# Kernel optimization log

Hardware: AMD Instinct MI355X
Metric: run time of the kernel (lower is better)

## Reference

```python
import jax, jax.numpy as jnp
import numpy as np

NEG_SLOPE = 0.1


def _conv3d(x, w, b):
    # standard 3x3x3 conv, stride 1, pad 1, NCDHW layout
    y = jax.lax.conv_general_dilated(
        x, w, window_strides=(1, 1, 1), padding=[(1, 1), (1, 1), (1, 1)],
        dimension_numbers=('NCDHW', 'OIDHW', 'NCDHW'))
    return y + b[None, :, None, None, None]


def _deform_conv3d_hw(x, w_off, b_off, w, b):
    """DeformConvPack_d with dimension='HW': 3x3x3 conv whose H/W sampling
    positions are shifted by learned per-location offsets (bilinear sample in
    H,W; integer taps in D). Zero padding outside the volume."""
    B, C, D, H, W = x.shape
    # offset conv: 2 offsets (dh, dw) per kernel tap, 27 taps -> 54 channels
    off = _conv3d(x, w_off, b_off).reshape(B, 27, 2, D, H, W)
    x_flat = x.reshape(B, C, D * H * W)
    d_grid = jnp.arange(D)[:, None, None]          # [D,1,1]
    h_grid = jnp.arange(H)[None, :, None]          # [1,H,1]
    w_grid = jnp.arange(W)[None, None, :]          # [1,1,W]
    out = jnp.zeros((B, w.shape[0], D, H, W), x.dtype)
    k = 0
    for kd in (-1, 0, 1):
        pd = d_grid + kd                            # integer depth tap
        valid_d = (pd >= 0) & (pd < D)
        pdc = jnp.clip(pd, 0, D - 1)
        for kh in (-1, 0, 1):
            for kw in (-1, 0, 1):
                ph = h_grid + kh + off[:, k, 0]     # [B,D,H,W] float
                pw = w_grid + kw + off[:, k, 1]
                h0 = jnp.floor(ph)
                w0 = jnp.floor(pw)
                th = ph - h0                        # bilinear fracs
                tw = pw - w0
                h0i = h0.astype(jnp.int32)
                w0i = w0.astype(jnp.int32)
                samp = jnp.zeros((B, C, D, H, W), x.dtype)
                for dh, wgt_h in ((0, 1.0 - th), (1, th)):
                    hh = h0i + dh
                    vh = (hh >= 0) & (hh < H)
                    hhc = jnp.clip(hh, 0, H - 1)
                    for dw, wgt_w in ((0, 1.0 - tw), (1, tw)):
                        ww = w0i + dw
                        v = valid_d & vh & (ww >= 0) & (ww < W)
                        wwc = jnp.clip(ww, 0, W - 1)
                        idx = (pdc * H + hhc) * W + wwc          # [B,D,H,W]
                        g = jnp.take_along_axis(
                            x_flat, idx.reshape(B, 1, D * H * W), axis=2
                        ).reshape(B, C, D, H, W)
                        wgt = jnp.where(v, wgt_h * wgt_w, 0.0)
                        samp = samp + g * wgt[:, None]
                # accumulate this tap's contribution through the conv weight
                out = out + jnp.einsum('bcdhw,oc->bodhw', samp,
                                       w[:, :, kd + 1, kh + 1, kw + 1])
                k += 1
    return out + b[None, :, None, None, None]


def setup_inputs() -> dict:
    key = jax.random.key(0)
    ks = jax.random.split(key, 9)
    B, nf, D, H, W = 4, 48, 12, 56, 56
    fan = 1.0 / np.sqrt(nf * 27)
    x = jax.random.normal(ks[0], (B, nf, D, H, W), jnp.float32)
    # offset convs: small weights so sampled offsets stay O(1) pixel
    w_off0 = jax.random.normal(ks[1], (54, nf, 3, 3, 3), jnp.float32) * 0.01
    b_off0 = jax.random.normal(ks[2], (54,), jnp.float32) * 0.01
    w0 = jax.random.normal(ks[3], (nf, nf, 3, 3, 3), jnp.float32) * fan
    b0 = jax.random.normal(ks[4], (nf,), jnp.float32) * 0.01
    w_off1 = jax.random.normal(ks[5], (54, nf, 3, 3, 3), jnp.float32) * 0.01
    b_off1 = jax.random.normal(ks[6], (54,), jnp.float32) * 0.01
    w1 = jax.random.normal(ks[7], (nf, nf, 3, 3, 3), jnp.float32) * fan
    b1 = jax.random.normal(ks[8], (nf,), jnp.float32) * 0.01
    return {"x": x, "w_off0": w_off0, "b_off0": b_off0, "w0": w0, "b0": b0,
            "w_off1": w_off1, "b_off1": b_off1, "w1": w1, "b1": b1}


def reference(x, w_off0, b_off0, w0, b0, w_off1, b_off1, w1, b1):
    h = _deform_conv3d_hw(x, w_off0, b_off0, w0, b0)
    h = jnp.where(h >= 0, h, NEG_SLOPE * h)  # LeakyReLU(0.1)
    y = _deform_conv3d_hw(h, w_off1, b_off1, w1, b1)
    return y + x
```

## Files before the change

kernel.cpp:

```cpp
#include <hip/hip_runtime.h>
#include <hip/hip_bf16.h>

constexpr int B_ = 4, C_ = 48, D_ = 12, H_ = 56, W_ = 56;
constexpr int DHW_ = D_ * H_ * W_;
constexpr int NLOC_ = B_ * DHW_;
constexpr int OFFC_ = 54;
constexpr int NXCD_ = 8;

typedef short bf16x8 __attribute__((ext_vector_type(8)));
typedef float f32x4  __attribute__((ext_vector_type(4)));
typedef float f32x2  __attribute__((ext_vector_type(2)));
typedef unsigned int u32x4 __attribute__((ext_vector_type(4)));
typedef unsigned int u32x2 __attribute__((ext_vector_type(2)));

__device__ __forceinline__ int xcd_swizzle(int bid, int nwg) {
    int xcd = bid % NXCD_, lid = bid / NXCD_;
    int q = nwg / NXCD_, r = nwg % NXCD_;
    return (xcd < r ? xcd * (q + 1) : r * (q + 1) + (xcd - r) * q) + lid;
}

__device__ __forceinline__ unsigned int f2bf_u(float f) {
    __hip_bfloat16 h = __float2bfloat16(f);
    return (unsigned int)__builtin_bit_cast(unsigned short, h);
}

__device__ __forceinline__ f32x2 bfpair(unsigned int pv) {
    f32x2 r;
    r.x = __builtin_bit_cast(float, pv << 16);
    r.y = __builtin_bit_cast(float, pv & 0xffff0000u);
    return r;
}
__device__ __forceinline__ f32x2 pk_mul(f32x2 a, f32x2 b) {
    f32x2 d;
    asm("v_pk_mul_f32 %0, %1, %2" : "=v"(d) : "v"(a), "v"(b));
    return d;
}
__device__ __forceinline__ f32x2 pk_fma(f32x2 a, f32x2 b, f32x2 c) {
    f32x2 d;
    asm("v_pk_fma_f32 %0, %1, %2, %3" : "=v"(d) : "v"(a), "v"(b), "v"(c));
    return d;
}
__device__ __forceinline__ unsigned int cvt_pk_bf16(float lo, float hi) {
    unsigned int r;
    asm("v_cvt_pk_bf16_f32 %0, %1, %2" : "=v"(r) : "v"(lo), "v"(hi));
    return r;
}

__device__ __forceinline__ u32x4 interp4_pk(u32x4 c00, u32x4 c01, u32x4 c10, u32x4 c11,
                                            f32x2 w0, f32x2 w1, f32x2 w2, f32x2 w3) {
    u32x4 pv;
#pragma unroll
    for (int u = 0; u < 4; ++u) {
        f32x2 r = pk_mul(w0, bfpair(c00[u]));
        r = pk_fma(w1, bfpair(c01[u]), r);
        r = pk_fma(w2, bfpair(c10[u]), r);
        r = pk_fma(w3, bfpair(c11[u]), r);
        pv[u] = cvt_pk_bf16(r.x, r.y);
    }
    return pv;
}

__global__ void __launch_bounds__(256) repack_frag_kernel(
    const float* __restrict__ w, unsigned short* __restrict__ wf, int OC, int MT) {
    int t = blockIdx.x * 256 + threadIdx.x;
    int total = 27 * MT * 1024;
    if (t >= total) return;
    int i    = t & 7;
    int lane = (t >> 3) & 63;
    int ks   = (t >> 9) & 1;
    int mt   = (t >> 10) % MT;
    int k    = t / (MT << 10);
    int oc = mt * 16 + (lane & 15);
    int c  = ks * 32 + 8 * (lane >> 4) + i;
    float v = (oc < OC && c < 48) ? w[((size_t)oc * 48 + c) * 27 + k] : 0.0f;
    wf[t] = (unsigned short)f2bf_u(v);
}

__global__ void __launch_bounds__(256) to_cl_kernel(const float* __restrict__ x,
                                                    unsigned short* __restrict__ xcl) {
    int loc = blockIdx.x * 256 + threadIdx.x;
    int b = loc / DHW_, s = loc - b * DHW_;
    const float* xp = x + (size_t)b * (C_ * DHW_) + s;
#pragma unroll
    for (int q = 0; q < 6; ++q) {
        float v[8];
#pragma unroll
        for (int u = 0; u < 8; ++u) v[u] = xp[(size_t)(q * 8 + u) * DHW_];
        u32x4 o;
#pragma unroll
        for (int u = 0; u < 4; ++u)
            o[u] = cvt_pk_bf16(v[2 * u], v[2 * u + 1]);
        *(u32x4*)(xcl + ((size_t)q * NLOC_ + loc) * 8) = o;
    }
}

__global__ void __launch_bounds__(128) offconv_mfma(
    const unsigned short* __restrict__ xcl,
    const unsigned short* __restrict__ wf,
    const float* __restrict__ bo,
    float* __restrict__ off) {
    __shared__ unsigned short S[2][64][64];
    int tid = threadIdx.x, wid = tid >> 6, lane = tid & 63;
    int base = xcd_swizzle(blockIdx.x, gridDim.x) * 64;
    int loc = base + lane;
    int b = loc / DHW_;
    int sp = loc - b * DHW_;
    int w = sp % W_; int t1 = sp / W_;
    int h = t1 % H_; int d = t1 / H_;
    int g = lane >> 4, li = lane & 15, l7 = lane & 7;

    u32x4 z = {0, 0, 0, 0};
    *(u32x4*)&S[wid][lane][(6 ^ l7) * 8] = z;
    *(u32x4*)&S[wid][lane][(7 ^ l7) * 8] = z;

    f32x4 acc[4][4];
#pragma unroll
    for (int mt = 0; mt < 4; ++mt)
#pragma unroll
        for (int nt = 0; nt < 4; ++nt) acc[mt][nt] = (f32x4){0.f, 0.f, 0.f, 0.f};

    const u32x4* plane[6];
#pragma unroll
    for (int q = 0; q < 6; ++q)
        plane[q] = (const u32x4*)(xcl + ((size_t)q * NLOC_ + (size_t)b * DHW_) * 8);

#pragma unroll 1
    for (int i = 0; i < 14; ++i) {
        int k = wid + 2 * i;
        if (k >= 27) break;
        int kd = k / 9 - 1, kh = (k / 3) % 3 - 1, kw = k % 3 - 1;
        int pd = d + kd, ph = h + kh, pw = w + kw;
        bool valid = (pd >= 0) & (pd < D_) & (ph >= 0) & (ph < H_) & (pw >= 0) & (pw < W_);
        int pdc = min(max(pd, 0), D_ - 1);
        int phc = min(max(ph, 0), H_ - 1);
        int pwc = min(max(pw, 0), W_ - 1);
        int pix = (pdc * H_ + phc) * W_ + pwc;
        u32x4 pv[6];
#pragma unroll
        for (int cc = 0; cc < 6; ++cc) pv[cc] = plane[cc][pix];
#pragma unroll
        for (int cc = 0; cc < 6; ++cc) {
            if (!valid) pv[cc] = z;
            *(u32x4*)&S[wid][lane][(cc ^ l7) * 8] = pv[cc];
        }
        const unsigned short* wk = wf + (size_t)k * 4096 + lane * 8;
        bf16x8 a[4][2];
#pragma unroll
        for (int mt = 0; mt < 4; ++mt)
#pragma unroll
            for (int ks = 0; ks < 2; ++ks)
                a[mt][ks] = *(const bf16x8*)&wk[(mt * 2 + ks) * 512];
#pragma unroll
        for (int nt = 0; nt < 4; ++nt) {
            const unsigned short* sr = &S[wid][nt * 16 + li][0];
            bf16x8 b0 = *(const bf16x8*)&sr[((0 + g) ^ l7) * 8];
            bf16x8 b1 = *(const bf16x8*)&sr[((4 + g) ^ l7) * 8];
#pragma unroll
            for (int mt = 0; mt < 4; ++mt) {
                acc[mt][nt] = __builtin_amdgcn_mfma_f32_16x16x32_bf16(a[mt][0], b0, acc[mt][nt], 0, 0, 0);
                acc[mt][nt] = __builtin_amdgcn_mfma_f32_16x16x32_bf16(a[mt][1], b1, acc[mt][nt], 0, 0, 0);
            }
        }
    }

    float* XCH = (float*)&S[0][0][0];
    __syncthreads();
    if (wid == 1) {
#pragma unroll
        for (int mt = 0; mt < 2; ++mt)
#pragma unroll
            for (int nt = 0; nt < 4; ++nt)
                *(f32x4*)(XCH + (mt * 4 + nt) * 256 + lane * 4) = acc[mt][nt];
    }
    __syncthreads();
    if (wid == 0) {
#pragma unroll
        for (int mt = 0; mt < 2; ++mt)
#pragma unroll
            for (int nt = 0; nt < 4; ++nt)
                acc[mt][nt] += *(f32x4*)(XCH + (mt * 4 + nt) * 256 + lane * 4);
    }
    __syncthreads();
    if (wid == 1) {
#pragma unroll
        for (int mt = 2; mt < 4; ++mt)
#pragma unroll
            for (int nt = 0; nt < 4; ++nt)
                *(f32x4*)(XCH + ((mt - 2) * 4 + nt) * 256 + lane * 4) = acc[mt][nt];
    }
    __syncthreads();
    if (wid == 1) return;
#pragma unroll
    for (int mt = 2; mt < 4; ++mt)
#pragma unroll
        for (int nt = 0; nt < 4; ++nt)
            acc[mt][nt] += *(f32x4*)(XCH + ((mt - 2) * 4 + nt) * 256 + lane * 4);

    int s0 = base - b * DHW_;
#pragma unroll
    for (int mt = 0; mt < 4; ++mt) {
#pragma unroll
        for (int r = 0; r < 4; ++r) {
            int oc = mt * 16 + 4 * g + r;
            if (oc < OFFC_) {
                float bb = bo[oc];
#pragma unroll
                for (int nt = 0; nt < 4; ++nt) {
                    size_t addr = ((size_t)b * OFFC_ + oc) * DHW_ + (s0 + nt * 16 + li);
                    off[addr] = acc[mt][nt][r] + bb;
                }
            }
        }
    }
}

template <int LEAKY, int RESID, int CLOUT>
__global__ void __launch_bounds__(128) deform_mfma(
    const unsigned short* __restrict__ scl,
    const float* __restrict__ off,
    const unsigned short* __restrict__ wf,
    const float* __restrict__ bias,
    const float* __restrict__ resid,
    float* __restrict__ dstf,
    unsigned short* __restrict__ dstcl) {
    __shared__ unsigned short S[2][64][64];
    int tid = threadIdx.x, wid = tid >> 6, lane = tid & 63;
    int base = xcd_swizzle(blockIdx.x, gridDim.x) * 64;
    int loc = base + lane;
    int b = loc / DHW_;
    int sp = loc - b * DHW_;
    int w = sp % W_; int t1 = sp / W_;
    int h = t1 % H_; int d = t1 / H_;
    int g = lane >> 4, li = lane & 15, l7 = lane & 7;

    u32x4 z = {0, 0, 0, 0};
    *(u32x4*)&S[wid][lane][(6 ^ l7) * 8] = z;
    *(u32x4*)&S[wid][lane][(7 ^ l7) * 8] = z;

    f32x4 acc[3][4];
#pragma unroll
    for (int mt = 0; mt < 3; ++mt)
#pragma unroll
        for (int nt = 0; nt < 4; ++nt) acc[mt][nt] = (f32x4){0.f, 0.f, 0.f, 0.f};

    const u32x4* plane[6];
#pragma unroll
    for (int q = 0; q < 6; ++q)
        plane[q] = (const u32x4*)(scl + ((size_t)q * NLOC_ + (size_t)b * DHW_) * 8);
    const float* ob = off + (size_t)b * (OFFC_ * DHW_) + sp;

#pragma unroll 1
    for (int i = 0; i < 14; ++i) {
        int k = wid + 2 * i;
        if (k >= 27) break;
        int kd = k / 9 - 1, kh = (k / 3) % 3 - 1, kw = k % 3 - 1;
        int pd = d + kd;
        bool vd = (pd >= 0) & (pd < D_);
        int pdc = min(max(pd, 0), D_ - 1);

        float odh = ob[(size_t)(2 * k + 0) * DHW_];
        float odw = ob[(size_t)(2 * k + 1) * DHW_];
        float phf = (float)(h + kh) + odh;
        float pwf = (float)(w + kw) + odw;
        float h0f = floorf(phf), w0f = floorf(pwf);
        float th = phf - h0f, tw = pwf - w0f;
        int h0 = (int)h0f, w0 = (int)w0f;

        int pix[4];
        f32x4 cw;
#pragma unroll
        for (int dh = 0; dh < 2; ++dh) {
            int hh = h0 + dh;
            bool vh = vd & (hh >= 0) & (hh < H_);
            int hhc = min(max(hh, 0), H_ - 1);
            float wh = dh ? th : 1.0f - th;
#pragma unroll
            for (int dw = 0; dw < 2; ++dw) {
                int ww = w0 + dw;
                bool v = vh & (ww >= 0) & (ww < W_);
                int wwc = min(max(ww, 0), W_ - 1);
                float wwt = dw ? tw : 1.0f - tw;
                pix[dh * 2 + dw] = (pdc * H_ + hhc) * W_ + wwc;
                cw[dh * 2 + dw] = v ? wh * wwt : 0.0f;
            }
        }
        f32x2 w0p = {cw[0], cw[0]}, w1p = {cw[1], cw[1]};
        f32x2 w2p = {cw[2], cw[2]}, w3p = {cw[3], cw[3]};

#pragma unroll
        for (int half = 0; half < 2; ++half) {
            u32x4 st[3][4];
#pragma unroll
            for (int cc = 0; cc < 3; ++cc)
#pragma unroll
                for (int j = 0; j < 4; ++j)
                    st[cc][j] = plane[half * 3 + cc][pix[j]];
#pragma unroll
            for (int cc = 0; cc < 3; ++cc) {
                u32x4 pv = interp4_pk(st[cc][0], st[cc][1], st[cc][2], st[cc][3],
                                      w0p, w1p, w2p, w3p);
                *(u32x4*)&S[wid][lane][((half * 3 + cc) ^ l7) * 8] = pv;
            }
        }

        const unsigned short* wk = wf + (size_t)k * 3072 + lane * 8;
        bf16x8 a[3][2];
#pragma unroll
        for (int mt = 0; mt < 3; ++mt)
#pragma unroll
            for (int ks = 0; ks < 2; ++ks)
                a[mt][ks] = *(const bf16x8*)&wk[(mt * 2 + ks) * 512];
#pragma unroll
        for (int nt = 0; nt < 4; ++nt) {
            const unsigned short* sr = &S[wid][nt * 16 + li][0];
            bf16x8 b0 = *(const bf16x8*)&sr[((0 + g) ^ l7) * 8];
            bf16x8 b1 = *(const bf16x8*)&sr[((4 + g) ^ l7) * 8];
#pragma unroll
            for (int mt = 0; mt < 3; ++mt) {
                acc[mt][nt] = __builtin_amdgcn_mfma_f32_16x16x32_bf16(a[mt][0], b0, acc[mt][nt], 0, 0, 0);
                acc[mt][nt] = __builtin_amdgcn_mfma_f32_16x16x32_bf16(a[mt][1], b1, acc[mt][nt], 0, 0, 0);
            }
        }
    }

    float* XCH = (float*)&S[1][0][0];
    __syncthreads();
    if (wid == 1) {
#pragma unroll
        for (int mt = 0; mt < 2; ++mt)
#pragma unroll
            for (int nt = 0; nt < 4; ++nt)
                *(f32x4*)(XCH + (mt * 4 + nt) * 256 + lane * 4) = acc[mt][nt];
    }
    __syncthreads();
    if (wid == 0) {
#pragma unroll
        for (int mt = 0; mt < 2; ++mt)
#pragma unroll
            for (int nt = 0; nt < 4; ++nt)
                acc[mt][nt] += *(f32x4*)(XCH + (mt * 4 + nt) * 256 + lane * 4);
    }
    __syncthreads();
    if (wid == 1) {
#pragma unroll
        for (int nt = 0; nt < 4; ++nt)
            *(f32x4*)(XCH + nt * 256 + lane * 4) = acc[2][nt];
    }
    __syncthreads();
    if (wid == 1) return;
#pragma unroll
    for (int nt = 0; nt < 4; ++nt)
        acc[2][nt] += *(f32x4*)(XCH + nt * 256 + lane * 4);

    if (CLOUT) {
        unsigned short* Sb = &S[0][0][0];
#pragma unroll
        for (int mt = 0; mt < 3; ++mt) {
#pragma unroll
            for (int nt = 0; nt < 4; ++nt) {
                float v[4];
#pragma unroll
                for (int r = 0; r < 4; ++r) {
                    int oc = mt * 16 + 4 * g + r;
                    float t = acc[mt][nt][r] + bias[oc];
                    if (LEAKY) t = (t >= 0.f) ? t : 0.1f * t;
                    v[r] = t;
                }
                int row = nt * 16 + li;
                int colb = (mt * 32 + 8 * g) ^ ((li & 7) << 4);
                u32x2 pp = {cvt_pk_bf16(v[0], v[1]), cvt_pk_bf16(v[2], v[3])};
                *(u32x2*)((char*)(Sb + (size_t)row * 64) + colb) = pp;
            }
        }
        unsigned short* myrow = Sb + (size_t)lane * 64;
#pragma unroll
        for (int s = 0; s < 6; ++s) {
            u32x4 c = *(u32x4*)((char*)myrow + ((s * 16) ^ ((lane & 7) << 4)));
            *(u32x4*)(dstcl + ((size_t)s * NLOC_ + loc) * 8) = c;
        }
    } else {
        int s0 = base - b * DHW_;
#pragma unroll
        for (int mt = 0; mt < 3; ++mt) {
#pragma unroll
            for (int r = 0; r < 4; ++r) {
                int oc = mt * 16 + 4 * g + r;
                float bb = bias[oc];
#pragma unroll
                for (int nt = 0; nt < 4; ++nt) {
                    size_t addr = ((size_t)b * C_ + oc) * DHW_ + (s0 + nt * 16 + li);
                    float v = acc[mt][nt][r] + bb;
                    if (LEAKY) v = (v >= 0.0f) ? v : 0.1f * v;
                    if (RESID) v += resid[addr];
                    dstf[addr] = v;
                }
            }
        }
    }
}

extern "C" void kernel_launch(void* const* d_in, const int* in_sizes, int n_in,
                              void* d_out, int out_size, void* d_ws, size_t ws_size,
                              hipStream_t stream) {
    const float* x      = (const float*)d_in[0];
    const float* w_off0 = (const float*)d_in[1];
    const float* b_off0 = (const float*)d_in[2];
    const float* w0     = (const float*)d_in[3];
    const float* b0     = (const float*)d_in[4];
    const float* w_off1 = (const float*)d_in[5];
    const float* b_off1 = (const float*)d_in[6];
    const float* w1     = (const float*)d_in[7];
    const float* b1     = (const float*)d_in[8];
    float* out = (float*)d_out;

    float* off_buf = (float*)d_ws;
    unsigned short* xcl = (unsigned short*)(off_buf + (size_t)OFFC_ * NLOC_);
    unsigned short* hcl = xcl + (size_t)NLOC_ * 48;
    unsigned short* wf_off  = hcl + (size_t)NLOC_ * 48;
    unsigned short* wf_conv = wf_off + 27 * 4 * 1024;

    dim3 blk128(128), blk256(256);
    int nblk = NLOC_ / 64;

    to_cl_kernel<<<NLOC_ / 256, blk256, 0, stream>>>(x, xcl);

    repack_frag_kernel<<<(27 * 4 * 1024 + 255) / 256, blk256, 0, stream>>>(w_off0, wf_off, OFFC_, 4);
    repack_frag_kernel<<<(27 * 3 * 1024 + 255) / 256, blk256, 0, stream>>>(w0, wf_conv, C_, 3);
    offconv_mfma<<<nblk, blk128, 0, stream>>>(xcl, wf_off, b_off0, off_buf);
    deform_mfma<1, 0, 1><<<nblk, blk128, 0, stream>>>(xcl, off_buf, wf_conv, b0, nullptr, nullptr, hcl);

    repack_frag_kernel<<<(27 * 4 * 1024 + 255) / 256, blk256, 0, stream>>>(w_off1, wf_off, OFFC_, 4);
    repack_frag_kernel<<<(27 * 3 * 1024 + 255) / 256, blk256, 0, stream>>>(w1, wf_conv, C_, 3);
    offconv_mfma<<<nblk, blk128, 0, stream>>>(hcl, wf_off, b_off1, off_buf);
    deform_mfma<0, 1, 0><<<nblk, blk128, 0, stream>>>(hcl, off_buf, wf_conv, b1, x, out, nullptr);
}
```

Before: 300.5 us.

## Halve per-block spatial tile to 32 locations, splitting channel gather across lane halves

```diff
diff --git a/kernel.cpp b/kernel.cpp
--- a/kernel.cpp
+++ b/kernel.cpp
@@ -99,30 +99,31 @@
     const unsigned short* __restrict__ wf,
     const float* __restrict__ bo,
     float* __restrict__ off) {
-    __shared__ unsigned short S[2][64][64];
+    __shared__ unsigned short S[2][32][64];
     int tid = threadIdx.x, wid = tid >> 6, lane = tid & 63;
-    int base = xcd_swizzle(blockIdx.x, gridDim.x) * 64;
-    int loc = base + lane;
+    int base = xcd_swizzle(blockIdx.x, gridDim.x) * 32;
+    int lh = lane & 31, cg = lane >> 5;
+    int loc = base + lh;
     int b = loc / DHW_;
     int sp = loc - b * DHW_;
     int w = sp % W_; int t1 = sp / W_;
     int h = t1 % H_; int d = t1 / H_;
     int g = lane >> 4, li = lane & 15, l7 = lane & 7;
+    int lh7 = lh & 7;
 
     u32x4 z = {0, 0, 0, 0};
-    *(u32x4*)&S[wid][lane][(6 ^ l7) * 8] = z;
-    *(u32x4*)&S[wid][lane][(7 ^ l7) * 8] = z;
-
-    f32x4 acc[4][4];
+    *(u32x4*)&S[wid][lh][(((6 + cg)) ^ lh7) * 8] = z;
+
+    f32x4 acc[4][2];
 #pragma unroll
     for (int mt = 0; mt < 4; ++mt)
 #pragma unroll
-        for (int nt = 0; nt < 4; ++nt) acc[mt][nt] = (f32x4){0.f, 0.f, 0.f, 0.f};
-
-    const u32x4* plane[6];
-#pragma unroll
-    for (int q = 0; q < 6; ++q)
-        plane[q] = (const u32x4*)(xcl + ((size_t)q * NLOC_ + (size_t)b * DHW_) * 8);
+        for (int nt = 0; nt < 2; ++nt) acc[mt][nt] = (f32x4){0.f, 0.f, 0.f, 0.f};
+
+    const u32x4* pl[3];
+#pragma unroll
+    for (int c = 0; c < 3; ++c)
+        pl[c] = (const u32x4*)(xcl + ((size_t)(3 * cg + c) * NLOC_ + (size_t)b * DHW_) * 8);
 
 #pragma unroll 1
     for (int i = 0; i < 14; ++i) {
@@ -135,13 +136,13 @@
         int phc = min(max(ph, 0), H_ - 1);
         int pwc = min(max(pw, 0), W_ - 1);
         int pix = (pdc * H_ + phc) * W_ + pwc;
-        u32x4 pv[6];
-#pragma unroll
-        for (int cc = 0; cc < 6; ++cc) pv[cc] = plane[cc][pix];
-#pragma unroll
-        for (int cc = 0; cc < 6; ++cc) {
-            if (!valid) pv[cc] = z;
-            *(u32x4*)&S[wid][lane][(cc ^ l7) * 8] = pv[cc];
+        u32x4 pv[3];
+#pragma unroll
+        for (int c = 0; c < 3; ++c) pv[c] = pl[c][pix];
+#pragma unroll
+        for (int c = 0; c < 3; ++c) {
+            if (!valid) pv[c] = z;
+            *(u32x4*)&S[wid][lh][((3 * cg + c) ^ lh7) * 8] = pv[c];
         }
         const unsigned short* wk = wf + (size_t)k * 4096 + lane * 8;
         bf16x8 a[4][2];
@@ -151,7 +152,7 @@
             for (int ks = 0; ks < 2; ++ks)
                 a[mt][ks] = *(const bf16x8*)&wk[(mt * 2 + ks) * 512];
 #pragma unroll
-        for (int nt = 0; nt < 4; ++nt) {
+        for (int nt = 0; nt < 2; ++nt) {
             const unsigned short* sr = &S[wid][nt * 16 + li][0];
             bf16x8 b0 = *(const bf16x8*)&sr[((0 + g) ^ l7) * 8];
             bf16x8 b1 = *(const bf16x8*)&sr[((4 + g) ^ l7) * 8];
@@ -167,34 +168,18 @@
     __syncthreads();
     if (wid == 1) {
 #pragma unroll
-        for (int mt = 0; mt < 2; ++mt)
-#pragma unroll
-            for (int nt = 0; nt < 4; ++nt)
-                *(f32x4*)(XCH + (mt * 4 + nt) * 256 + lane * 4) = acc[mt][nt];
-    }
-    __syncthreads();
-    if (wid == 0) {
-#pragma unroll
-        for (int mt = 0; mt < 2; ++mt)
-#pragma unroll
-            for (int nt = 0; nt < 4; ++nt)
-                acc[mt][nt] += *(f32x4*)(XCH + (mt * 4 + nt) * 256 + lane * 4);
-    }
-    __syncthreads();
-    if (wid == 1) {
-#pragma unroll
-        for (int mt = 2; mt < 4; ++mt)
-#pragma unroll
-            for (int nt = 0; nt < 4; ++nt)
-                *(f32x4*)(XCH + ((mt - 2) * 4 + nt) * 256 + lane * 4) = acc[mt][nt];
+        for (int mt = 0; mt < 4; ++mt)
+#pragma unroll
+            for (int nt = 0; nt < 2; ++nt)
+                *(f32x4*)(XCH + (mt * 2 + nt) * 256 + lane * 4) = acc[mt][nt];
     }
     __syncthreads();
     if (wid == 1) return;
 #pragma unroll
-    for (int mt = 2; mt < 4; ++mt)
-#pragma unroll
-        for (int nt = 0; nt < 4; ++nt)
-            acc[mt][nt] += *(f32x4*)(XCH + ((mt - 2) * 4 + nt) * 256 + lane * 4);
+    for (int mt = 0; mt < 4; ++mt)
+#pragma unroll
+        for (int nt = 0; nt < 2; ++nt)
+            acc[mt][nt] += *(f32x4*)(XCH + (mt * 2 + nt) * 256 + lane * 4);
 
     int s0 = base - b * DHW_;
 #pragma unroll
@@ -205,7 +190,7 @@
             if (oc < OFFC_) {
                 float bb = bo[oc];
 #pragma unroll
-                for (int nt = 0; nt < 4; ++nt) {
+                for (int nt = 0; nt < 2; ++nt) {
                     size_t addr = ((size_t)b * OFFC_ + oc) * DHW_ + (s0 + nt * 16 + li);
                     off[addr] = acc[mt][nt][r] + bb;
                 }
@@ -223,30 +208,31 @@
     const float* __restrict__ resid,
     float* __restrict__ dstf,
     unsigned short* __restrict__ dstcl) {
-    __shared__ unsigned short S[2][64][64];
+    __shared__ unsigned short S[2][32][64];
     int tid = threadIdx.x, wid = tid >> 6, lane = tid & 63;
-    int base = xcd_swizzle(blockIdx.x, gridDim.x) * 64;
-    int loc = base + lane;
+    int base = xcd_swizzle(blockIdx.x, gridDim.x) * 32;
+    int lh = lane & 31, cg = lane >> 5;
+    int loc = base + lh;
     int b = loc / DHW_;
     int sp = loc - b * DHW_;
     int w = sp % W_; int t1 = sp / W_;
     int h = t1 % H_; int d = t1 / H_;
     int g = lane >> 4, li = lane & 15, l7 = lane & 7;
+    int lh7 = lh & 7;
 
     u32x4 z = {0, 0, 0, 0};
-    *(u32x4*)&S[wid][lane][(6 ^ l7) * 8] = z;
-    *(u32x4*)&S[wid][lane][(7 ^ l7) * 8] = z;
-
-    f32x4 acc[3][4];
+    *(u32x4*)&S[wid][lh][(((6 + cg)) ^ lh7) * 8] = z;
+
+    f32x4 acc[3][2];
 #pragma unroll
     for (int mt = 0; mt < 3; ++mt)
 #pragma unroll
-        for (int nt = 0; nt < 4; ++nt) acc[mt][nt] = (f32x4){0.f, 0.f, 0.f, 0.f};
-
-    const u32x4* plane[6];
-#pragma unroll
-    for (int q = 0; q < 6; ++q)
-        plane[q] = (const u32x4*)(scl + ((size_t)q * NLOC_ + (size_t)b * DHW_) * 8);
+        for (int nt = 0; nt < 2; ++nt) acc[mt][nt] = (f32x4){0.f, 0.f, 0.f, 0.f};
+
+    const u32x4* pl[3];
+#pragma unroll
+    for (int c = 0; c < 3; ++c)
+        pl[c] = (const u32x4*)(scl + ((size_t)(3 * cg + c) * NLOC_ + (size_t)b * DHW_) * 8);
     const float* ob = off + (size_t)b * (OFFC_ * DHW_) + sp;
 
 #pragma unroll 1
@@ -287,20 +273,17 @@
         f32x2 w0p = {cw[0], cw[0]}, w1p = {cw[1], cw[1]};
         f32x2 w2p = {cw[2], cw[2]}, w3p = {cw[3], cw[3]};
 
-#pragma unroll
-        for (int half = 0; half < 2; ++half) {
-            u32x4 st[3][4];
-#pragma unroll
-            for (int cc = 0; cc < 3; ++cc)
-#pragma unroll
-                for (int j = 0; j < 4; ++j)
-                    st[cc][j] = plane[half * 3 + cc][pix[j]];
-#pragma unroll
-            for (int cc = 0; cc < 3; ++cc) {
-                u32x4 pv = interp4_pk(st[cc][0], st[cc][1], st[cc][2], st[cc][3],
-                                      w0p, w1p, w2p, w3p);
-                *(u32x4*)&S[wid][lane][((half * 3 + cc) ^ l7) * 8] = pv;
-            }
+        u32x4 st[3][4];
+#pragma unroll
+        for (int c = 0; c < 3; ++c)
+#pragma unroll
+            for (int j = 0; j < 4; ++j)
+                st[c][j] = pl[c][pix[j]];
+#pragma unroll
+        for (int c = 0; c < 3; ++c) {
+            u32x4 pv = interp4_pk(st[c][0], st[c][1], st[c][2], st[c][3],
+                                  w0p, w1p, w2p, w3p);
+            *(u32x4*)&S[wid][lh][((3 * cg + c) ^ lh7) * 8] = pv;
         }
 
         const unsigned short* wk = wf + (size_t)k * 3072 + lane * 8;
@@ -311,7 +294,7 @@
             for (int ks = 0; ks < 2; ++ks)
                 a[mt][ks] = *(const bf16x8*)&wk[(mt * 2 + ks) * 512];
 #pragma unroll
-        for (int nt = 0; nt < 4; ++nt) {
+        for (int nt = 0; nt < 2; ++nt) {
             const unsigned short* sr = &S[wid][nt * 16 + li][0];
             bf16x8 b0 = *(const bf16x8*)&sr[((0 + g) ^ l7) * 8];
             bf16x8 b1 = *(const bf16x8*)&sr[((4 + g) ^ l7) * 8];
@@ -323,41 +306,29 @@
         }
     }
 
-    float* XCH = (float*)&S[1][0][0];
+    float* XCH = (float*)&S[0][0][0];
     __syncthreads();
     if (wid == 1) {
 #pragma unroll
-        for (int mt = 0; mt < 2; ++mt)
-#pragma unroll
-            for (int nt = 0; nt < 4; ++nt)
-                *(f32x4*)(XCH + (mt * 4 + nt) * 256 + lane * 4) = acc[mt][nt];
-    }
-    __syncthreads();
-    if (wid == 0) {
-#pragma unroll
-        for (int mt = 0; mt < 2; ++mt)
-#pragma unroll
-            for (int nt = 0; nt < 4; ++nt)
-                acc[mt][nt] += *(f32x4*)(XCH + (mt * 4 + nt) * 256 + lane * 4);
-    }
-    __syncthreads();
-    if (wid == 1) {
-#pragma unroll
-        for (int nt = 0; nt < 4; ++nt)
-            *(f32x4*)(XCH + nt * 256 + lane * 4) = acc[2][nt];
+        for (int mt = 0; mt < 3; ++mt)
+#pragma unroll
+            for (int nt = 0; nt < 2; ++nt)
+                *(f32x4*)(XCH + (mt * 2 + nt) * 256 + lane * 4) = acc[mt][nt];
     }
     __syncthreads();
     if (wid == 1) return;
 #pragma unroll
-    for (int nt = 0; nt < 4; ++nt)
-        acc[2][nt] += *(f32x4*)(XCH + nt * 256 + lane * 4);
+    for (int mt = 0; mt < 3; ++mt)
+#pragma unroll
+        for (int nt = 0; nt < 2; ++nt)
+            acc[mt][nt] += *(f32x4*)(XCH + (mt * 2 + nt) * 256 + lane * 4);
 
     if (CLOUT) {
         unsigned short* Sb = &S[0][0][0];
 #pragma unroll
         for (int mt = 0; mt < 3; ++mt) {
 #pragma unroll
-            for (int nt = 0; nt < 4; ++nt) {
+            for (int nt = 0; nt < 2; ++nt) {
                 float v[4];
 #pragma unroll
                 for (int r = 0; r < 4; ++r) {
@@ -372,11 +343,12 @@
                 *(u32x2*)((char*)(Sb + (size_t)row * 64) + colb) = pp;
             }
         }
-        unsigned short* myrow = Sb + (size_t)lane * 64;
-#pragma unroll
-        for (int s = 0; s < 6; ++s) {
-            u32x4 c = *(u32x4*)((char*)myrow + ((s * 16) ^ ((lane & 7) << 4)));
-            *(u32x4*)(dstcl + ((size_t)s * NLOC_ + loc) * 8) = c;
+        unsigned short* myrow = Sb + (size_t)lh * 64;
+#pragma unroll
+        for (int c = 0; c < 3; ++c) {
+            int s = 3 * cg + c;
+            u32x4 cc = *(u32x4*)((char*)myrow + ((s * 16) ^ (lh7 << 4)));
+            *(u32x4*)(dstcl + ((size_t)s * NLOC_ + base + lh) * 8) = cc;
         }
     } else {
         int s0 = base - b * DHW_;
@@ -387,7 +359,7 @@
                 int oc = mt * 16 + 4 * g + r;
                 float bb = bias[oc];
 #pragma unroll
-                for (int nt = 0; nt < 4; ++nt) {
+                for (int nt = 0; nt < 2; ++nt) {
                     size_t addr = ((size_t)b * C_ + oc) * DHW_ + (s0 + nt * 16 + li);
                     float v = acc[mt][nt][r] + bb;
                     if (LEAKY) v = (v >= 0.0f) ? v : 0.1f * v;
@@ -420,7 +392,7 @@
     unsigned short* wf_conv = wf_off + 27 * 4 * 1024;
 
     dim3 blk128(128), blk256(256);
-    int nblk = NLOC_ / 64;
+    int nblk = NLOC_ / 32;
 
     to_cl_kernel<<<NLOC_ / 256, blk256, 0, stream>>>(x, xcl);
 
```

After: 333.7 us. +11.0%, slower.

## Software-pipeline gather loads one tap ahead of MFMA in conv kernels

Applied to the files above, without the earlier changes.

```diff
diff --git a/kernel.cpp b/kernel.cpp
--- a/kernel.cpp
+++ b/kernel.cpp
@@ -124,24 +124,37 @@
     for (int q = 0; q < 6; ++q)
         plane[q] = (const u32x4*)(xcl + ((size_t)q * NLOC_ + (size_t)b * DHW_) * 8);
 
-#pragma unroll 1
-    for (int i = 0; i < 14; ++i) {
-        int k = wid + 2 * i;
-        if (k >= 27) break;
+    int k = wid;
+    u32x4 pv[6];
+    bool valid;
+    {
         int kd = k / 9 - 1, kh = (k / 3) % 3 - 1, kw = k % 3 - 1;
         int pd = d + kd, ph = h + kh, pw = w + kw;
-        bool valid = (pd >= 0) & (pd < D_) & (ph >= 0) & (ph < H_) & (pw >= 0) & (pw < W_);
-        int pdc = min(max(pd, 0), D_ - 1);
-        int phc = min(max(ph, 0), H_ - 1);
-        int pwc = min(max(pw, 0), W_ - 1);
-        int pix = (pdc * H_ + phc) * W_ + pwc;
-        u32x4 pv[6];
+        valid = (pd >= 0) & (pd < D_) & (ph >= 0) & (ph < H_) & (pw >= 0) & (pw < W_);
+        int pix = (min(max(pd, 0), D_ - 1) * H_ + min(max(ph, 0), H_ - 1)) * W_
+                  + min(max(pw, 0), W_ - 1);
 #pragma unroll
         for (int cc = 0; cc < 6; ++cc) pv[cc] = plane[cc][pix];
+    }
+
+#pragma unroll 1
+    for (;;) {
+        int kn = k + 2;
+        bool have_next = (kn < 27);
 #pragma unroll
         for (int cc = 0; cc < 6; ++cc) {
-            if (!valid) pv[cc] = z;
-            *(u32x4*)&S[wid][lane][(cc ^ l7) * 8] = pv[cc];
+            u32x4 t = valid ? pv[cc] : z;
+            *(u32x4*)&S[wid][lane][(cc ^ l7) * 8] = t;
+        }
+        bool validn = false;
+        if (have_next) {
+            int kd = kn / 9 - 1, kh = (kn / 3) % 3 - 1, kw = kn % 3 - 1;
+            int pd = d + kd, ph = h + kh, pw = w + kw;
+            validn = (pd >= 0) & (pd < D_) & (ph >= 0) & (ph < H_) & (pw >= 0) & (pw < W_);
+            int pix = (min(max(pd, 0), D_ - 1) * H_ + min(max(ph, 0), H_ - 1)) * W_
+                      + min(max(pw, 0), W_ - 1);
+#pragma unroll
+            for (int cc = 0; cc < 6; ++cc) pv[cc] = plane[cc][pix];
         }
         const unsigned short* wk = wf + (size_t)k * 4096 + lane * 8;
         bf16x8 a[4][2];
@@ -161,6 +174,9 @@
                 acc[mt][nt] = __builtin_amdgcn_mfma_f32_16x16x32_bf16(a[mt][1], b1, acc[mt][nt], 0, 0, 0);
             }
         }
+        if (!have_next) break;
+        k = kn;
+        valid = validn;
     }
 
     float* XCH = (float*)&S[0][0][0];
@@ -249,23 +265,22 @@
         plane[q] = (const u32x4*)(scl + ((size_t)q * NLOC_ + (size_t)b * DHW_) * 8);
     const float* ob = off + (size_t)b * (OFFC_ * DHW_) + sp;
 
-#pragma unroll 1
-    for (int i = 0; i < 14; ++i) {
-        int k = wid + 2 * i;
-        if (k >= 27) break;
+    int k = wid;
+    u32x4 st[6][4];
+    f32x2 wp0, wp1, wp2, wp3;
+    float odh_n = 0.f, odw_n = 0.f;
+    {
+        float odh = ob[(size_t)(2 * k + 0) * DHW_];
+        float odw = ob[(size_t)(2 * k + 1) * DHW_];
         int kd = k / 9 - 1, kh = (k / 3) % 3 - 1, kw = k % 3 - 1;
         int pd = d + kd;
         bool vd = (pd >= 0) & (pd < D_);
         int pdc = min(max(pd, 0), D_ - 1);
-
-        float odh = ob[(size_t)(2 * k + 0) * DHW_];
-        float odw = ob[(size_t)(2 * k + 1) * DHW_];
         float phf = (float)(h + kh) + odh;
         float pwf = (float)(w + kw) + odw;
         float h0f = floorf(phf), w0f = floorf(pwf);
         float th = phf - h0f, tw = pwf - w0f;
         int h0 = (int)h0f, w0 = (int)w0f;
-
         int pix[4];
         f32x4 cw;
 #pragma unroll
@@ -273,7 +288,7 @@
             int hh = h0 + dh;
             bool vh = vd & (hh >= 0) & (hh < H_);
             int hhc = min(max(hh, 0), H_ - 1);
-            float wh = dh ? th : 1.0f - th;
+            float whv = dh ? th : 1.0f - th;
 #pragma unroll
             for (int dw = 0; dw < 2; ++dw) {
                 int ww = w0 + dw;
@@ -281,28 +296,71 @@
                 int wwc = min(max(ww, 0), W_ - 1);
                 float wwt = dw ? tw : 1.0f - tw;
                 pix[dh * 2 + dw] = (pdc * H_ + hhc) * W_ + wwc;
-                cw[dh * 2 + dw] = v ? wh * wwt : 0.0f;
-            }
-        }
-        f32x2 w0p = {cw[0], cw[0]}, w1p = {cw[1], cw[1]};
-        f32x2 w2p = {cw[2], cw[2]}, w3p = {cw[3], cw[3]};
-
-#pragma unroll
-        for (int half = 0; half < 2; ++half) {
-            u32x4 st[3][4];
-#pragma unroll
-            for (int cc = 0; cc < 3; ++cc)
-#pragma unroll
-                for (int j = 0; j < 4; ++j)
-                    st[cc][j] = plane[half * 3 + cc][pix[j]];
-#pragma unroll
-            for (int cc = 0; cc < 3; ++cc) {
-                u32x4 pv = interp4_pk(st[cc][0], st[cc][1], st[cc][2], st[cc][3],
-                                      w0p, w1p, w2p, w3p);
-                *(u32x4*)&S[wid][lane][((half * 3 + cc) ^ l7) * 8] = pv;
-            }
-        }
-
+                cw[dh * 2 + dw] = v ? whv * wwt : 0.0f;
+            }
+        }
+        wp0 = (f32x2){cw[0], cw[0]}; wp1 = (f32x2){cw[1], cw[1]};
+        wp2 = (f32x2){cw[2], cw[2]}; wp3 = (f32x2){cw[3], cw[3]};
+#pragma unroll
+        for (int cc = 0; cc < 6; ++cc)
+#pragma unroll
+            for (int j = 0; j < 4; ++j) st[cc][j] = plane[cc][pix[j]];
+        if (k + 2 < 27) {
+            odh_n = ob[(size_t)(2 * (k + 2) + 0) * DHW_];
+            odw_n = ob[(size_t)(2 * (k + 2) + 1) * DHW_];
+        }
+    }
+
+#pragma unroll 1
+    for (;;) {
+        int kn = k + 2;
+        bool have_next = (kn < 27);
+        float odh_nn = 0.f, odw_nn = 0.f;
+        if (kn + 2 < 27) {
+            odh_nn = ob[(size_t)(2 * (kn + 2) + 0) * DHW_];
+            odw_nn = ob[(size_t)(2 * (kn + 2) + 1) * DHW_];
+        }
+#pragma unroll
+        for (int cc = 0; cc < 6; ++cc) {
+            u32x4 pvv = interp4_pk(st[cc][0], st[cc][1], st[cc][2], st[cc][3],
+                                   wp0, wp1, wp2, wp3);
+            *(u32x4*)&S[wid][lane][(cc ^ l7) * 8] = pvv;
+        }
+        if (have_next) {
+            int kd = kn / 9 - 1, kh = (kn / 3) % 3 - 1, kw = kn % 3 - 1;
+            int pd = d + kd;
+            bool vd = (pd >= 0) & (pd < D_);
+            int pdc = min(max(pd, 0), D_ - 1);
+            float phf = (float)(h + kh) + odh_n;
+            float pwf = (float)(w + kw) + odw_n;
+            float h0f = floorf(phf), w0f = floorf(pwf);
+            float th = phf - h0f, tw = pwf - w0f;
+            int h0 = (int)h0f, w0 = (int)w0f;
+            int pix[4];
+            f32x4 cw;
+#pragma unroll
+            for (int dh = 0; dh < 2; ++dh) {
+                int hh = h0 + dh;
+                bool vh = vd & (hh >= 0) & (hh < H_);
+                int hhc = min(max(hh, 0), H_ - 1);
+                float whv = dh ? th : 1.0f - th;
+#pragma unroll
+                for (int dw = 0; dw < 2; ++dw) {
+                    int ww = w0 + dw;
+                    bool v = vh & (ww >= 0) & (ww < W_);
+                    int wwc = min(max(ww, 0), W_ - 1);
+                    float wwt = dw ? tw : 1.0f - tw;
+                    pix[dh * 2 + dw] = (pdc * H_ + hhc) * W_ + wwc;
+                    cw[dh * 2 + dw] = v ? whv * wwt : 0.0f;
+                }
+            }
+            wp0 = (f32x2){cw[0], cw[0]}; wp1 = (f32x2){cw[1], cw[1]};
+            wp2 = (f32x2){cw[2], cw[2]}; wp3 = (f32x2){cw[3], cw[3]};
+#pragma unroll
+            for (int cc = 0; cc < 6; ++cc)
+#pragma unroll
+                for (int j = 0; j < 4; ++j) st[cc][j] = plane[cc][pix[j]];
+        }
         const unsigned short* wk = wf + (size_t)k * 3072 + lane * 8;
         bf16x8 a[3][2];
 #pragma unroll
@@ -321,6 +379,10 @@
                 acc[mt][nt] = __builtin_amdgcn_mfma_f32_16x16x32_bf16(a[mt][1], b1, acc[mt][nt], 0, 0, 0);
             }
         }
+        if (!have_next) break;
+        k = kn;
+        odh_n = odh_nn;
+        odw_n = odw_nn;
     }
 
     float* XCH = (float*)&S[1][0][0];
```

Result: slower. 338.5 us (+12.6%).
